# Kernel optimization log

Measured on AMD Instinct MI355X. Metric: run time of the kernel, lower is better.

## Reference

```python
import jax, jax.numpy as jnp
import numpy as np

SCALE_FACTOR = 8.0  # sqrt(head_dim=64)
GAMMA = 1.0
NEG_INF = -1e9


def setup_inputs() -> dict:
    key = jax.random.key(0)
    kq, kk, kv, km = jax.random.split(key, 4)
    B, H, S, D = 4, 16, 2048, 64
    q = jax.random.normal(kq, (B, H, S, D), dtype=jnp.float32)
    k = jax.random.normal(kk, (B, H, S, D), dtype=jnp.float32)
    v = jax.random.normal(kv, (B, H, S, D), dtype=jnp.float32)
    mask = jax.random.randint(km, (B, 1, S, S), 0, 2, dtype=jnp.int32)
    return {"q": q, "k": k, "v": v, "mask": mask}


def reference(q, k, v, mask):
    # attn = (q/scale) @ k^T, masked, softmax along last dim, scaled by gamma
    scores = jnp.einsum("bhsd,bhtd->bhst", q / SCALE_FACTOR, k)  # [B,H,S,S]
    scores = jnp.where(mask == 0, NEG_INF, scores)
    attn = jax.nn.softmax(scores, axis=-1) * GAMMA
    output = jnp.einsum("bhst,bhtd->bhsd", attn, v) + v  # AV + residual V
    return (output, attn)
```

## Files before the change

### kernel.cpp

```cpp
#include <hip/hip_runtime.h>

typedef _Float16 f16;
typedef _Float16 f16x4 __attribute__((ext_vector_type(4)));
typedef _Float16 f16x8 __attribute__((ext_vector_type(8)));
typedef float f32x16 __attribute__((ext_vector_type(16)));

#define MFMA16(a, b, c) __builtin_amdgcn_mfma_f32_32x32x16_f16((a), (b), (c), 0, 0, 0)

constexpr int B_ = 4, H_ = 16, S_ = 2048, D_ = 64;
constexpr int QB = 128;
constexpr int WQ = 32;
constexpr int KB = 64;
constexpr int NKT = S_ / KB;
constexpr size_t OUT0 = (size_t)B_ * H_ * S_ * D_;

__device__ __forceinline__ int swzb(int row, int col ) {
  int byte = (row << 7) + (col << 1);
  return byte ^ ((row & 7) << 4);
}

__global__ __launch_bounds__(256) void attn_fused(
    const float* __restrict__ qg_, const float* __restrict__ kg_,
    const float* __restrict__ vg_, const int* __restrict__ mg_,
    float* __restrict__ out) {
  __shared__ f16 Kl[KB * D_];
  __shared__ f16 Vt[D_ * KB];
  __shared__ f16 Pl[4 * WQ * KB];

  const int tid = threadIdx.x;
  const int lane = tid & 63;
  const int wid = tid >> 6;
  const int ln = lane & 31;
  const int hi = lane >> 5;

  const int bh = blockIdx.y;
  const int b = bh >> 4;
  const int qb = blockIdx.x * QB + wid * WQ;

  const float* qg = qg_ + (size_t)bh * S_ * D_;
  const float* kg = kg_ + (size_t)bh * S_ * D_;
  const float* vg = vg_ + (size_t)bh * S_ * D_;
  const int* mg = mg_ + (size_t)b * S_ * S_;
  float* outp = out + (size_t)bh * S_ * D_;
  float* attnp = out + OUT0 + (size_t)bh * S_ * S_;

  char* KlB = (char*)Kl;
  char* VtB = (char*)Vt;
  char* PlB = (char*)Pl + wid * (WQ * KB * 2);

  f16x8 qf[4];
  {
    const float* qrow = qg + (size_t)(qb + ln) * D_;
#pragma unroll
    for (int s = 0; s < 4; ++s) {
      const int d0 = s * 16 + hi * 8;
      float4 a = *(const float4*)(qrow + d0);
      float4 c = *(const float4*)(qrow + d0 + 4);
      f16x8 t;
      t[0] = (f16)(a.x * 0.125f); t[1] = (f16)(a.y * 0.125f);
      t[2] = (f16)(a.z * 0.125f); t[3] = (f16)(a.w * 0.125f);
      t[4] = (f16)(c.x * 0.125f); t[5] = (f16)(c.y * 0.125f);
      t[6] = (f16)(c.z * 0.125f); t[7] = (f16)(c.w * 0.125f);
      qf[s] = t;
    }
  }

  float rsum[16];
#pragma unroll
  for (int r = 0; r < 16; ++r) rsum[r] = 0.0f;

  for (int kt = 0; kt < NKT; ++kt) {
    __syncthreads();
#pragma unroll
    for (int rep = 0; rep < 4; ++rep) {
      const int idx = (rep * 256 + tid) * 4;
      const int row = idx >> 6, col = idx & 63;
      float4 x = *(const float4*)(kg + (size_t)(kt * KB + row) * D_ + col);
      f16x4 hx = {(f16)x.x, (f16)x.y, (f16)x.z, (f16)x.w};
      *(f16x4*)(KlB + swzb(row, col)) = hx;
    }
    __syncthreads();
#pragma unroll
    for (int sub = 0; sub < 2; ++sub) {
      f32x16 sacc;
#pragma unroll
      for (int i = 0; i < 16; ++i) sacc[i] = 0.0f;
#pragma unroll
      for (int s = 0; s < 4; ++s) {
        f16x8 kf = *(const f16x8*)(KlB + swzb(sub * 32 + ln, s * 16 + hi * 8));
        sacc = MFMA16(qf[s], kf, sacc);
      }
      const int t0 = kt * KB + sub * 32;
      const int* mrow = mg + (size_t)(qb + 4 * hi) * S_ + t0 + ln;
#pragma unroll
      for (int r = 0; r < 16; ++r) {
        const int qoff = (r & 3) + 8 * (r >> 2);
        const int m = mrow[(size_t)qoff * S_];
        rsum[r] += (m != 0) ? __expf(sacc[r]) : 0.0f;
      }
    }
  }

  float rinv[16];
#pragma unroll
  for (int r = 0; r < 16; ++r) {
    float s = rsum[r];
    s += __shfl_xor(s, 16);
    s += __shfl_xor(s, 8);
    s += __shfl_xor(s, 4);
    s += __shfl_xor(s, 2);
    s += __shfl_xor(s, 1);
    rinv[r] = 1.0f / s;
  }

  f32x16 oacc0, oacc1;
#pragma unroll
  for (int i = 0; i < 16; ++i) { oacc0[i] = 0.0f; oacc1[i] = 0.0f; }

  for (int kt = 0; kt < NKT; ++kt) {
    __syncthreads();
#pragma unroll
    for (int rep = 0; rep < 4; ++rep) {
      const int idx = (rep * 256 + tid) * 4;
      const int row = idx >> 6, col = idx & 63;
      float4 x = *(const float4*)(kg + (size_t)(kt * KB + row) * D_ + col);
      f16x4 hx = {(f16)x.x, (f16)x.y, (f16)x.z, (f16)x.w};
      *(f16x4*)(KlB + swzb(row, col)) = hx;
      float4 y = *(const float4*)(vg + (size_t)(kt * KB + row) * D_ + col);
      *(f16*)(VtB + swzb(col + 0, row)) = (f16)y.x;
      *(f16*)(VtB + swzb(col + 1, row)) = (f16)y.y;
      *(f16*)(VtB + swzb(col + 2, row)) = (f16)y.z;
      *(f16*)(VtB + swzb(col + 3, row)) = (f16)y.w;
    }
    __syncthreads();
#pragma unroll
    for (int sub = 0; sub < 2; ++sub) {
      f32x16 sacc;
#pragma unroll
      for (int i = 0; i < 16; ++i) sacc[i] = 0.0f;
#pragma unroll
      for (int s = 0; s < 4; ++s) {
        f16x8 kf = *(const f16x8*)(KlB + swzb(sub * 32 + ln, s * 16 + hi * 8));
        sacc = MFMA16(qf[s], kf, sacc);
      }
      const int t0 = kt * KB + sub * 32;
      const int* mrow = mg + (size_t)(qb + 4 * hi) * S_ + t0 + ln;
      float* arow = attnp + (size_t)(qb + 4 * hi) * S_ + t0 + ln;
#pragma unroll
      for (int r = 0; r < 16; ++r) {
        const int qoff = (r & 3) + 8 * (r >> 2);
        const int m = mrow[(size_t)qoff * S_];
        float p = (m != 0) ? __expf(sacc[r]) * rinv[r] : 0.0f;
        arow[(size_t)qoff * S_] = p;
        *(f16*)(PlB + swzb(qoff + 4 * hi, sub * 32 + ln)) = (f16)p;
      }
    }
#pragma unroll
    for (int ts = 0; ts < 4; ++ts) {
      f16x8 pa = *(const f16x8*)(PlB + swzb(ln, ts * 16 + hi * 8));
      f16x8 vb0 = *(const f16x8*)(VtB + swzb(ln, ts * 16 + hi * 8));
      f16x8 vb1 = *(const f16x8*)(VtB + swzb(32 + ln, ts * 16 + hi * 8));
      oacc0 = MFMA16(pa, vb0, oacc0);
      oacc1 = MFMA16(pa, vb1, oacc1);
    }
  }

#pragma unroll
  for (int r = 0; r < 16; ++r) {
    const int qoff = (r & 3) + 8 * (r >> 2);
    const size_t o = (size_t)(qb + qoff + 4 * hi) * D_ + ln;
    outp[o] = oacc0[r] + vg[o];
    outp[o + 32] = oacc1[r] + vg[o + 32];
  }
}

extern "C" void kernel_launch(void* const* d_in, const int* in_sizes, int n_in,
                              void* d_out, int out_size, void* d_ws, size_t ws_size,
                              hipStream_t stream) {
  (void)in_sizes; (void)n_in; (void)out_size; (void)d_ws; (void)ws_size;
  const float* q = (const float*)d_in[0];
  const float* k = (const float*)d_in[1];
  const float* v = (const float*)d_in[2];
  const int* mask = (const int*)d_in[3];
  float* out = (float*)d_out;
  dim3 grid(S_ / QB, B_ * H_);
  attn_fused<<<grid, dim3(256), 0, stream>>>(q, k, v, mask, out);
}
```

Before: 2.201 ms.

## Split attention into key-split rowsum, attn-emit, and output kernels

Replaces the single fused kernel with four launches: zeroing a workspace, computing softmax row sums with the key dimension split four ways and combined through atomics, writing the attention matrix in a separate split-key kernel, and computing the AV output in its own kernel. This raises parallelism beyond the 1024-block grid and adds register prefetch of K/V tiles. In exchange QK^T and the mask reads are now done three times instead of twice, and the attention and output passes no longer share work.

```diff
diff --git a/kernel.cpp b/kernel.cpp
--- a/kernel.cpp
+++ b/kernel.cpp
@@ -7,10 +7,13 @@
 
 #define MFMA16(a, b, c) __builtin_amdgcn_mfma_f32_32x32x16_f16((a), (b), (c), 0, 0, 0)
 
-constexpr int B_ = 4, H_ = 16, S_ = 2048, D_ = 64;
+constexpr int B_ = 4, H_ = 16, S_ = 2048, D_ = 64, BH = 64;
 constexpr int QB = 128;
 constexpr int WQ = 32;
 constexpr int KB = 64;
+constexpr int TS = 512;
+constexpr int NSPLIT = S_ / TS;
+constexpr int NKT_W = TS / KB;
 constexpr int NKT = S_ / KB;
 constexpr size_t OUT0 = (size_t)B_ * H_ * S_ * D_;
 
@@ -19,139 +22,237 @@
   return byte ^ ((row & 7) << 4);
 }
 
-__global__ __launch_bounds__(256) void attn_fused(
+__device__ __forceinline__ void kload256(const float* g, int kt, int tid, float4 kr[4]) {
+#pragma unroll
+  for (int rep = 0; rep < 4; ++rep) {
+    int idx = (rep * 256 + tid) * 4;
+    kr[rep] = *(const float4*)(g + (size_t)(kt * KB + (idx >> 6)) * D_ + (idx & 63));
+  }
+}
+__device__ __forceinline__ void kwrite256(char* KlB, int tid, const float4 kr[4]) {
+#pragma unroll
+  for (int rep = 0; rep < 4; ++rep) {
+    int idx = (rep * 256 + tid) * 4;
+    f16x4 hx = {(f16)kr[rep].x, (f16)kr[rep].y, (f16)kr[rep].z, (f16)kr[rep].w};
+    *(f16x4*)(KlB + swzb(idx >> 6, idx & 63)) = hx;
+  }
+}
+__device__ __forceinline__ void vwrite256(char* VtB, int tid, const float4 vr[4]) {
+#pragma unroll
+  for (int rep = 0; rep < 4; ++rep) {
+    int idx = (rep * 256 + tid) * 4;
+    int row = idx >> 6, col = idx & 63;
+    *(f16*)(VtB + swzb(col + 0, row)) = (f16)vr[rep].x;
+    *(f16*)(VtB + swzb(col + 1, row)) = (f16)vr[rep].y;
+    *(f16*)(VtB + swzb(col + 2, row)) = (f16)vr[rep].z;
+    *(f16*)(VtB + swzb(col + 3, row)) = (f16)vr[rep].w;
+  }
+}
+
+__device__ __forceinline__ void load_qf(const float* qg, int qrow, int hi, f16x8 qf[4]) {
+  const float* qr = qg + (size_t)qrow * D_;
+#pragma unroll
+  for (int s = 0; s < 4; ++s) {
+    const int d0 = s * 16 + hi * 8;
+    float4 a = *(const float4*)(qr + d0);
+    float4 c = *(const float4*)(qr + d0 + 4);
+    f16x8 t;
+    t[0] = (f16)(a.x * 0.125f); t[1] = (f16)(a.y * 0.125f);
+    t[2] = (f16)(a.z * 0.125f); t[3] = (f16)(a.w * 0.125f);
+    t[4] = (f16)(c.x * 0.125f); t[5] = (f16)(c.y * 0.125f);
+    t[6] = (f16)(c.z * 0.125f); t[7] = (f16)(c.w * 0.125f);
+    qf[s] = t;
+  }
+}
+
+__device__ __forceinline__ f32x16 qk8(const char* KlB, const f16x8 qf[4], int sub, int ln, int hi) {
+  f32x16 s;
+#pragma unroll
+  for (int i = 0; i < 16; ++i) s[i] = 0.0f;
+#pragma unroll
+  for (int t = 0; t < 4; ++t) {
+    f16x8 kf = *(const f16x8*)(KlB + swzb(sub * 32 + ln, t * 16 + hi * 8));
+    s = MFMA16(qf[t], kf, s);
+  }
+  return s;
+}
+
+__global__ void zero_ws(float* __restrict__ p, int n) {
+  int i = blockIdx.x * blockDim.x + threadIdx.x;
+  if (i < n) p[i] = 0.0f;
+}
+
+__global__ __launch_bounds__(256, 4) void attn_rsum(
+    const float* __restrict__ qg_, const float* __restrict__ kg_,
+    const int* __restrict__ mg_, float* __restrict__ ws) {
+  __shared__ f16 Kl[KB * D_];
+  const int tid = threadIdx.x, lane = tid & 63, wid = tid >> 6;
+  const int ln = lane & 31, hi = lane >> 5;
+  const int bh = blockIdx.z, b = bh >> 4;
+  const int qb = blockIdx.x * QB + wid * WQ;
+  const int kt0 = blockIdx.y * NKT_W;
+  const float* qg = qg_ + (size_t)bh * S_ * D_;
+  const float* kg = kg_ + (size_t)bh * S_ * D_;
+  const int* mg = mg_ + (size_t)b * S_ * S_;
+  char* KlB = (char*)Kl;
+
+  f16x8 qf[4];
+  load_qf(qg, qb + ln, hi, qf);
+  float rs[16];
+#pragma unroll
+  for (int r = 0; r < 16; ++r) rs[r] = 0.0f;
+
+  float4 kr[4];
+  kload256(kg, kt0, tid, kr);
+  for (int i = 0; i < NKT_W; ++i) {
+    __syncthreads();
+    kwrite256(KlB, tid, kr);
+    if (i + 1 < NKT_W) kload256(kg, kt0 + i + 1, tid, kr);
+    __syncthreads();
+#pragma unroll
+    for (int sub = 0; sub < 2; ++sub) {
+      const int t0 = (kt0 + i) * KB + sub * 32;
+      const int* mrow = mg + (size_t)(qb + 4 * hi) * S_ + t0 + ln;
+      int mk[16];
+#pragma unroll
+      for (int r = 0; r < 16; ++r) {
+        const int qoff = (r & 3) + 8 * (r >> 2);
+        mk[r] = mrow[(size_t)qoff * S_];
+      }
+      f32x16 sacc = qk8(KlB, qf, sub, ln, hi);
+#pragma unroll
+      for (int r = 0; r < 16; ++r) rs[r] += mk[r] ? __expf(sacc[r]) : 0.0f;
+    }
+  }
+  float* wsrow = ws + (size_t)bh * S_;
+#pragma unroll
+  for (int r = 0; r < 16; ++r) {
+    float s = rs[r];
+    s += __shfl_xor(s, 16); s += __shfl_xor(s, 8); s += __shfl_xor(s, 4);
+    s += __shfl_xor(s, 2); s += __shfl_xor(s, 1);
+    if (ln == 0) {
+      const int qoff = (r & 3) + 8 * (r >> 2);
+      atomicAdd(wsrow + qb + qoff + 4 * hi, s);
+    }
+  }
+}
+
+__global__ __launch_bounds__(256, 4) void attn_emit(
+    const float* __restrict__ qg_, const float* __restrict__ kg_,
+    const int* __restrict__ mg_, const float* __restrict__ ws,
+    float* __restrict__ out) {
+  __shared__ f16 Kl[KB * D_];
+  const int tid = threadIdx.x, lane = tid & 63, wid = tid >> 6;
+  const int ln = lane & 31, hi = lane >> 5;
+  const int bh = blockIdx.z, b = bh >> 4;
+  const int qb = blockIdx.x * QB + wid * WQ;
+  const int kt0 = blockIdx.y * NKT_W;
+  const float* qg = qg_ + (size_t)bh * S_ * D_;
+  const float* kg = kg_ + (size_t)bh * S_ * D_;
+  const int* mg = mg_ + (size_t)b * S_ * S_;
+  float* attnp = out + OUT0 + (size_t)bh * S_ * S_;
+  char* KlB = (char*)Kl;
+
+  f16x8 qf[4];
+  load_qf(qg, qb + ln, hi, qf);
+  const float* wsrow = ws + (size_t)bh * S_;
+  float rinv[16];
+#pragma unroll
+  for (int r = 0; r < 16; ++r) {
+    const int qoff = (r & 3) + 8 * (r >> 2);
+    rinv[r] = 1.0f / wsrow[qb + qoff + 4 * hi];
+  }
+
+  float4 kr[4];
+  kload256(kg, kt0, tid, kr);
+  for (int i = 0; i < NKT_W; ++i) {
+    __syncthreads();
+    kwrite256(KlB, tid, kr);
+    if (i + 1 < NKT_W) kload256(kg, kt0 + i + 1, tid, kr);
+    __syncthreads();
+#pragma unroll
+    for (int sub = 0; sub < 2; ++sub) {
+      const int t0 = (kt0 + i) * KB + sub * 32;
+      const int* mrow = mg + (size_t)(qb + 4 * hi) * S_ + t0 + ln;
+      int mk[16];
+#pragma unroll
+      for (int r = 0; r < 16; ++r) {
+        const int qoff = (r & 3) + 8 * (r >> 2);
+        mk[r] = mrow[(size_t)qoff * S_];
+      }
+      f32x16 sacc = qk8(KlB, qf, sub, ln, hi);
+      float* arow = attnp + (size_t)(qb + 4 * hi) * S_ + t0 + ln;
+#pragma unroll
+      for (int r = 0; r < 16; ++r) {
+        const int qoff = (r & 3) + 8 * (r >> 2);
+        float p = mk[r] ? __expf(sacc[r]) * rinv[r] : 0.0f;
+        arow[(size_t)qoff * S_] = p;
+      }
+    }
+  }
+}
+
+__global__ __launch_bounds__(256) void attn_out(
     const float* __restrict__ qg_, const float* __restrict__ kg_,
     const float* __restrict__ vg_, const int* __restrict__ mg_,
-    float* __restrict__ out) {
+    const float* __restrict__ ws, float* __restrict__ out) {
   __shared__ f16 Kl[KB * D_];
   __shared__ f16 Vt[D_ * KB];
   __shared__ f16 Pl[4 * WQ * KB];
-
-  const int tid = threadIdx.x;
-  const int lane = tid & 63;
-  const int wid = tid >> 6;
-  const int ln = lane & 31;
-  const int hi = lane >> 5;
-
-  const int bh = blockIdx.y;
-  const int b = bh >> 4;
+  const int tid = threadIdx.x, lane = tid & 63, wid = tid >> 6;
+  const int ln = lane & 31, hi = lane >> 5;
+  const int bh = blockIdx.y, b = bh >> 4;
   const int qb = blockIdx.x * QB + wid * WQ;
-
   const float* qg = qg_ + (size_t)bh * S_ * D_;
   const float* kg = kg_ + (size_t)bh * S_ * D_;
   const float* vg = vg_ + (size_t)bh * S_ * D_;
   const int* mg = mg_ + (size_t)b * S_ * S_;
   float* outp = out + (size_t)bh * S_ * D_;
-  float* attnp = out + OUT0 + (size_t)bh * S_ * S_;
-
   char* KlB = (char*)Kl;
   char* VtB = (char*)Vt;
   char* PlB = (char*)Pl + wid * (WQ * KB * 2);
 
   f16x8 qf[4];
-  {
-    const float* qrow = qg + (size_t)(qb + ln) * D_;
-#pragma unroll
-    for (int s = 0; s < 4; ++s) {
-      const int d0 = s * 16 + hi * 8;
-      float4 a = *(const float4*)(qrow + d0);
-      float4 c = *(const float4*)(qrow + d0 + 4);
-      f16x8 t;
-      t[0] = (f16)(a.x * 0.125f); t[1] = (f16)(a.y * 0.125f);
-      t[2] = (f16)(a.z * 0.125f); t[3] = (f16)(a.w * 0.125f);
-      t[4] = (f16)(c.x * 0.125f); t[5] = (f16)(c.y * 0.125f);
-      t[6] = (f16)(c.z * 0.125f); t[7] = (f16)(c.w * 0.125f);
-      qf[s] = t;
-    }
-  }
-
-  float rsum[16];
-#pragma unroll
-  for (int r = 0; r < 16; ++r) rsum[r] = 0.0f;
-
+  load_qf(qg, qb + ln, hi, qf);
+  const float* wsrow = ws + (size_t)bh * S_;
+  float rinv[16];
+#pragma unroll
+  for (int r = 0; r < 16; ++r) {
+    const int qoff = (r & 3) + 8 * (r >> 2);
+    rinv[r] = 1.0f / wsrow[qb + qoff + 4 * hi];
+  }
+
+  f32x16 oacc0, oacc1;
+#pragma unroll
+  for (int i = 0; i < 16; ++i) { oacc0[i] = 0.0f; oacc1[i] = 0.0f; }
+
+  float4 kr[4], vr[4];
+  kload256(kg, 0, tid, kr);
+  kload256(vg, 0, tid, vr);
   for (int kt = 0; kt < NKT; ++kt) {
     __syncthreads();
-#pragma unroll
-    for (int rep = 0; rep < 4; ++rep) {
-      const int idx = (rep * 256 + tid) * 4;
-      const int row = idx >> 6, col = idx & 63;
-      float4 x = *(const float4*)(kg + (size_t)(kt * KB + row) * D_ + col);
-      f16x4 hx = {(f16)x.x, (f16)x.y, (f16)x.z, (f16)x.w};
-      *(f16x4*)(KlB + swzb(row, col)) = hx;
+    kwrite256(KlB, tid, kr);
+    vwrite256(VtB, tid, vr);
+    if (kt + 1 < NKT) {
+      kload256(kg, kt + 1, tid, kr);
+      kload256(vg, kt + 1, tid, vr);
     }
     __syncthreads();
 #pragma unroll
     for (int sub = 0; sub < 2; ++sub) {
-      f32x16 sacc;
-#pragma unroll
-      for (int i = 0; i < 16; ++i) sacc[i] = 0.0f;
-#pragma unroll
-      for (int s = 0; s < 4; ++s) {
-        f16x8 kf = *(const f16x8*)(KlB + swzb(sub * 32 + ln, s * 16 + hi * 8));
-        sacc = MFMA16(qf[s], kf, sacc);
-      }
       const int t0 = kt * KB + sub * 32;
       const int* mrow = mg + (size_t)(qb + 4 * hi) * S_ + t0 + ln;
-#pragma unroll
-      for (int r = 0; r < 16; ++r) {
-        const int qoff = (r & 3) + 8 * (r >> 2);
-        const int m = mrow[(size_t)qoff * S_];
-        rsum[r] += (m != 0) ? __expf(sacc[r]) : 0.0f;
-      }
-    }
-  }
-
-  float rinv[16];
-#pragma unroll
-  for (int r = 0; r < 16; ++r) {
-    float s = rsum[r];
-    s += __shfl_xor(s, 16);
-    s += __shfl_xor(s, 8);
-    s += __shfl_xor(s, 4);
-    s += __shfl_xor(s, 2);
-    s += __shfl_xor(s, 1);
-    rinv[r] = 1.0f / s;
-  }
-
-  f32x16 oacc0, oacc1;
-#pragma unroll
-  for (int i = 0; i < 16; ++i) { oacc0[i] = 0.0f; oacc1[i] = 0.0f; }
-
-  for (int kt = 0; kt < NKT; ++kt) {
-    __syncthreads();
-#pragma unroll
-    for (int rep = 0; rep < 4; ++rep) {
-      const int idx = (rep * 256 + tid) * 4;
-      const int row = idx >> 6, col = idx & 63;
-      float4 x = *(const float4*)(kg + (size_t)(kt * KB + row) * D_ + col);
-      f16x4 hx = {(f16)x.x, (f16)x.y, (f16)x.z, (f16)x.w};
-      *(f16x4*)(KlB + swzb(row, col)) = hx;
-      float4 y = *(const float4*)(vg + (size_t)(kt * KB + row) * D_ + col);
-      *(f16*)(VtB + swzb(col + 0, row)) = (f16)y.x;
-      *(f16*)(VtB + swzb(col + 1, row)) = (f16)y.y;
-      *(f16*)(VtB + swzb(col + 2, row)) = (f16)y.z;
-      *(f16*)(VtB + swzb(col + 3, row)) = (f16)y.w;
-    }
-    __syncthreads();
-#pragma unroll
-    for (int sub = 0; sub < 2; ++sub) {
-      f32x16 sacc;
-#pragma unroll
-      for (int i = 0; i < 16; ++i) sacc[i] = 0.0f;
-#pragma unroll
-      for (int s = 0; s < 4; ++s) {
-        f16x8 kf = *(const f16x8*)(KlB + swzb(sub * 32 + ln, s * 16 + hi * 8));
-        sacc = MFMA16(qf[s], kf, sacc);
-      }
-      const int t0 = kt * KB + sub * 32;
-      const int* mrow = mg + (size_t)(qb + 4 * hi) * S_ + t0 + ln;
-      float* arow = attnp + (size_t)(qb + 4 * hi) * S_ + t0 + ln;
-#pragma unroll
-      for (int r = 0; r < 16; ++r) {
-        const int qoff = (r & 3) + 8 * (r >> 2);
-        const int m = mrow[(size_t)qoff * S_];
-        float p = (m != 0) ? __expf(sacc[r]) * rinv[r] : 0.0f;
-        arow[(size_t)qoff * S_] = p;
+      int mk[16];
+#pragma unroll
+      for (int r = 0; r < 16; ++r) {
+        const int qoff = (r & 3) + 8 * (r >> 2);
+        mk[r] = mrow[(size_t)qoff * S_];
+      }
+      f32x16 sacc = qk8(KlB, qf, sub, ln, hi);
+#pragma unroll
+      for (int r = 0; r < 16; ++r) {
+        const int qoff = (r & 3) + 8 * (r >> 2);
+        float p = mk[r] ? __expf(sacc[r]) * rinv[r] : 0.0f;
         *(f16*)(PlB + swzb(qoff + 4 * hi, sub * 32 + ln)) = (f16)p;
       }
     }
@@ -177,12 +278,17 @@
 extern "C" void kernel_launch(void* const* d_in, const int* in_sizes, int n_in,
                               void* d_out, int out_size, void* d_ws, size_t ws_size,
                               hipStream_t stream) {
-  (void)in_sizes; (void)n_in; (void)out_size; (void)d_ws; (void)ws_size;
+  (void)in_sizes; (void)n_in; (void)out_size; (void)ws_size;
   const float* q = (const float*)d_in[0];
   const float* k = (const float*)d_in[1];
   const float* v = (const float*)d_in[2];
   const int* mask = (const int*)d_in[3];
   float* out = (float*)d_out;
-  dim3 grid(S_ / QB, B_ * H_);
-  attn_fused<<<grid, dim3(256), 0, stream>>>(q, k, v, mask, out);
-}
+  float* wsf = (float*)d_ws;
+
+  const int nsum = BH * S_;
+  zero_ws<<<dim3((nsum + 255) / 256), dim3(256), 0, stream>>>(wsf, nsum);
+  attn_rsum<<<dim3(S_ / QB, NSPLIT, BH), dim3(256), 0, stream>>>(q, k, mask, wsf);
+  attn_emit<<<dim3(S_ / QB, NSPLIT, BH), dim3(256), 0, stream>>>(q, k, mask, wsf, out);
+  attn_out<<<dim3(S_ / QB, BH), dim3(256), 0, stream>>>(q, k, v, mask, wsf, out);
+}
```

Measured after the change: 2.154 ms. 2.2% less time.
